# Optimization experiments

Hardware: AMD Instinct MI355X
Metric: run time of the kernel (lower is better)

Reference implementation:

```python
import jax, jax.numpy as jnp
import numpy as np

N_NODES = 65536
N_EDGES = 1048576
BN_EPS = 1e-5


def _glorot(key, shape):
    fan_in, fan_out = shape[0], shape[1]
    lim = np.sqrt(6.0 / (fan_in + fan_out))
    return jax.random.uniform(key, shape, jnp.float32, -lim, lim)


def setup_inputs() -> dict:
    key = jax.random.key(0)
    ks = jax.random.split(key, 16)
    inp = {}
    inp['x'] = jax.random.normal(ks[0], (N_NODES, 3), jnp.float32)
    inp['edge_src'] = jax.random.randint(ks[1], (N_EDGES,), 0, N_NODES, jnp.int32)
    inp['edge_dst'] = jax.random.randint(ks[2], (N_EDGES,), 0, N_NODES, jnp.int32)
    inp['edge_val'] = jax.random.uniform(ks[3], (N_EDGES,), jnp.float32)
    inp['num_pts'] = 1024  # points per shape (equal-size split)
    # GraphConvolution params: out = adj @ (x @ W) + b
    inp['gc1_w'] = _glorot(ks[4], (3, 64));     inp['gc1_b'] = jnp.zeros((64,), jnp.float32)
    inp['gc2_w'] = _glorot(ks[5], (64, 64));    inp['gc2_b'] = jnp.zeros((64,), jnp.float32)
    inp['gc3_w'] = _glorot(ks[6], (64, 1024));  inp['gc3_b'] = jnp.zeros((1024,), jnp.float32)
    # MLP head: Linear(1024,512)+BN+ReLU, Linear(512,256)+BN+ReLU, Linear(256,40)
    inp['fc1_w'] = _glorot(ks[7], (1024, 512)); inp['fc1_b'] = jnp.zeros((512,), jnp.float32)
    inp['bn1_g'] = jnp.ones((512,), jnp.float32); inp['bn1_b'] = jnp.zeros((512,), jnp.float32)
    inp['fc2_w'] = _glorot(ks[8], (512, 256));  inp['fc2_b'] = jnp.zeros((256,), jnp.float32)
    inp['bn2_g'] = jnp.ones((256,), jnp.float32); inp['bn2_b'] = jnp.zeros((256,), jnp.float32)
    inp['fc3_w'] = _glorot(ks[9], (256, 40));   inp['fc3_b'] = jnp.zeros((40,), jnp.float32)
    return inp


def _gcn_layer(x, w, b, src, dst, val):
    # adj @ (x @ W) + b, adj given as COO edge list (dst <- src weighted by val)
    support = x @ w                                   # [N, F_out]
    msg = support[src] * val[:, None]                 # gather + scale
    agg = jax.ops.segment_sum(msg, dst, num_segments=N_NODES)
    return agg + b


def _batchnorm(x, gamma, beta):
    mean = jnp.mean(x, axis=0)
    var = jnp.mean(jnp.square(x - mean), axis=0)  # biased var (torch train mode)
    return (x - mean) * jax.lax.rsqrt(var + BN_EPS) * gamma + beta


def reference(x, edge_src, edge_dst, edge_val, num_pts,
              gc1_w, gc1_b, gc2_w, gc2_b, gc3_w, gc3_b,
              fc1_w, fc1_b, bn1_g, bn1_b, fc2_w, fc2_b, bn2_g, bn2_b, fc3_w, fc3_b):
    h = jax.nn.relu(_gcn_layer(x, gc1_w, gc1_b, edge_src, edge_dst, edge_val))
    h = jax.nn.relu(_gcn_layer(h, gc2_w, gc2_b, edge_src, edge_dst, edge_val))
    h = jax.nn.relu(_gcn_layer(h, gc3_w, gc3_b, edge_src, edge_dst, edge_val))
    # per-shape max pool: split into equal-size shapes along node dim
    n_shapes = N_NODES // num_pts
    global_feat = jnp.max(h.reshape(n_shapes, num_pts, 1024), axis=1)  # [B, 1024]
    # MLP head with train-mode BatchNorm
    z = jax.nn.relu(_batchnorm(global_feat @ fc1_w + fc1_b, bn1_g, bn1_b))
    z = jax.nn.relu(_batchnorm(z @ fc2_w + fc2_b, bn2_g, bn2_b))
    scores = z @ fc3_w + fc3_b                         # [B, 40]
    return jax.nn.log_softmax(scores, axis=-1)
```

## Files before the change

### kernel.cpp

```cpp
#include <hip/hip_runtime.h>
#include <math.h>

#define NN 65536
#define NE 1048576
#define CAP 17408
#define PCAP 24576

typedef __attribute__((ext_vector_type(8))) short short8;
typedef __attribute__((ext_vector_type(4))) float f32x4;

__device__ inline unsigned short f2bf(float f) {
  unsigned u = __float_as_uint(f);
  unsigned r = u + 0x7fff + ((u >> 16) & 1);
  return (unsigned short)(r >> 16);
}
__device__ inline float bf2f(unsigned short h) { return __uint_as_float(((unsigned)h) << 16); }

__global__ __launch_bounds__(256) void k_prep(const float* __restrict__ x, float4* __restrict__ x4,
                                              int* __restrict__ gcur, const float* __restrict__ w3,
                                              unsigned short* __restrict__ bfrag, unsigned* __restrict__ gf) {
  int bid = blockIdx.x, tid = threadIdx.x;
  if (bid < 256) {
    if (bid == 0 && tid < 64) gcur[tid] = 0;
    int n = bid * 256 + tid;
    x4[n] = make_float4(x[3 * n], x[3 * n + 1], x[3 * n + 2], 0.f);
  } else {
    int t = (bid - 256) * 256 + tid;
    if (t < 65536) gf[t] = 0u;
    int e = t & 7, g = (t >> 3) & 3, col = (t >> 5) & 1023, q = t >> 15;
    int k = (q & 1) * 32 + g * 8 + e;
    float v = w3[k * 1024 + col];
    unsigned short hv = f2bf(v);
    bfrag[t] = (q < 2) ? hv : f2bf(v - bf2f(hv));
  }
}

__global__ __launch_bounds__(256) void k_bin(const int* __restrict__ src, const int* __restrict__ dst,
                                             const float* __restrict__ val, int* __restrict__ gcur,
                                             uint2* __restrict__ ebin) {
  __shared__ int cnt[64], base[64];
  int tid = threadIdx.x;
  if (tid < 64) cnt[tid] = 0;
  __syncthreads();
  int e0 = blockIdx.x * 4096;
  int rsrc[16], rdst[16], rrank[16];
  float rval[16];
#pragma unroll
  for (int i = 0; i < 16; ++i) {
    int e = e0 + i * 256 + tid;
    rsrc[i] = src[e];
    rdst[i] = dst[e];
    rval[i] = val[e];
    rrank[i] = atomicAdd(&cnt[rdst[i] >> 10], 1);
  }
  __syncthreads();
  if (tid < 64) base[tid] = atomicAdd(&gcur[tid], cnt[tid]);
  __syncthreads();
#pragma unroll
  for (int i = 0; i < 16; ++i) {
    int b = rdst[i] >> 10;
    ebin[b * CAP + base[b] + rrank[i]] =
        make_uint2((unsigned)rsrc[i] | ((unsigned)(rdst[i] & 1023) << 16), (unsigned)__float_as_int(rval[i]));
  }
}

__global__ __launch_bounds__(1024) void k_csr(const int* __restrict__ gcnt, const uint2* __restrict__ ebin,
                                              int2* __restrict__ offdeg, int2* __restrict__ pack) {
  __shared__ int lcnt[1024], lcur[1024], part[1024];
  int b = blockIdx.x, tid = threadIdx.x;
  int count = gcnt[b];
  int gbase = b * PCAP;
  lcnt[tid] = 0;
  __syncthreads();
  const uint2* eb = ebin + (size_t)b * CAP;
  for (int i0 = 0; i0 < count; i0 += 4096) {
    unsigned xs[4];
#pragma unroll
    for (int u = 0; u < 4; ++u) {
      int i = i0 + u * 1024 + tid;
      xs[u] = eb[min(i, count - 1)].x;
    }
#pragma unroll
    for (int u = 0; u < 4; ++u) {
      int i = i0 + u * 1024 + tid;
      if (i < count) atomicAdd(&lcnt[(xs[u] >> 16) & 1023], 1);
    }
  }
  __syncthreads();
  int deg = lcnt[tid];
  int pdeg = (deg + 7) & ~7;
  part[tid] = pdeg;
  __syncthreads();
  for (int d = 1; d < 1024; d <<= 1) {
    int v = (tid >= d) ? part[tid - d] : 0;
    __syncthreads();
    part[tid] += v;
    __syncthreads();
  }
  int o0 = part[tid] - pdeg;
  lcur[tid] = o0;
  offdeg[b * 1024 + tid] = make_int2(gbase + o0, pdeg);
  __syncthreads();
  for (int i0 = 0; i0 < count; i0 += 4096) {
    uint2 es[4];
#pragma unroll
    for (int u = 0; u < 4; ++u) {
      int i = i0 + u * 1024 + tid;
      es[u] = eb[min(i, count - 1)];
    }
#pragma unroll
    for (int u = 0; u < 4; ++u) {
      int i = i0 + u * 1024 + tid;
      if (i < count) {
        int ld = (es[u].x >> 16) & 1023;
        int p = atomicAdd(&lcur[ld], 1);
        pack[gbase + p] = make_int2((int)((es[u].x & 0xffffu) << 7), (int)es[u].y);
      }
    }
  }
  int pend = o0 + pdeg;
  for (int p = o0 + deg; p < pend; ++p) pack[gbase + p] = make_int2(0, 0);
}

__global__ __launch_bounds__(256) void k_aggx(const int2* __restrict__ offdeg, const int2* __restrict__ pack,
                                              const float4* __restrict__ x4, float* __restrict__ aggx) {
  int n = blockIdx.x * 256 + threadIdx.x;
  int2 od = offdeg[n];
  int i0 = od.x, pdeg = od.y;
  float a0 = 0.f, a1 = 0.f, a2 = 0.f;
  for (int b = 0; b < pdeg; b += 8) {
    int2 ed[8];
    float4 q[8];
#pragma unroll
    for (int u = 0; u < 8; ++u) ed[u] = pack[i0 + b + u];
#pragma unroll
    for (int u = 0; u < 8; ++u) q[u] = x4[(unsigned)ed[u].x >> 7];
#pragma unroll
    for (int u = 0; u < 8; ++u) {
      float v = __int_as_float(ed[u].y);
      a0 = fmaf(v, q[u].x, a0);
      a1 = fmaf(v, q[u].y, a1);
      a2 = fmaf(v, q[u].z, a2);
    }
  }
  aggx[n * 3 + 0] = a0;
  aggx[n * 3 + 1] = a1;
  aggx[n * 3 + 2] = a2;
}

__global__ __launch_bounds__(256) void k_gemm1(const float* __restrict__ aggx, const float* __restrict__ w,
                                               const float* __restrict__ b, unsigned short* __restrict__ out) {
  __shared__ float sw[256];
  int t = threadIdx.x;
  sw[t] = (t < 192) ? w[t] : b[t - 192];
  __syncthreads();
  int g = blockIdx.x * 256 + t;
  int n = g >> 6, j = g & 63;
  float a0 = aggx[n * 3], a1 = aggx[n * 3 + 1], a2 = aggx[n * 3 + 2];
  float r = sw[192 + j];
  r = fmaf(a0, sw[j], r);
  r = fmaf(a1, sw[64 + j], r);
  r = fmaf(a2, sw[128 + j], r);
  out[g] = f2bf(fmaxf(r, 0.f));
}

__global__ __launch_bounds__(256) void k_agg64g2(const int2* __restrict__ offdeg, const int2* __restrict__ pack,
                                                 const unsigned short* __restrict__ h,
                                                 const float* __restrict__ w2, const float* __restrict__ b2,
                                                 unsigned short* __restrict__ out) {
  __shared__ float sw[64][64];
  __shared__ float rows[32][64];
  int tid = threadIdx.x;
  int lane = tid & 63, wv = tid >> 6;
  for (int t = tid; t < 1024; t += 256) ((float4*)sw)[t] = ((const float4*)w2)[t];
  __syncthreads();
  int o = lane >> 3, fl = lane & 7;
  int n = blockIdx.x * 32 + wv * 8 + o;
  int2 od = offdeg[n];
  int i0 = od.x, pdeg = od.y;
  const char* hb = (const char*)h;
  unsigned fo = (unsigned)(fl << 4);
  float c0 = 0.f, c1 = 0.f, c2 = 0.f, c3 = 0.f, c4 = 0.f, c5 = 0.f, c6 = 0.f, c7 = 0.f;
  for (int b = 0; b < pdeg; b += 8) {
    int2 ed[8];
    uint4 hv[8];
#pragma unroll
    for (int u = 0; u < 8; ++u) ed[u] = pack[i0 + b + u];
#pragma unroll
    for (int u = 0; u < 8; ++u) hv[u] = *(const uint4*)(hb + ((unsigned)ed[u].x + fo));
#pragma unroll
    for (int u = 0; u < 8; ++u) {
      float v = __int_as_float(ed[u].y);
      c0 = fmaf(v, __uint_as_float(hv[u].x << 16), c0);
      c1 = fmaf(v, __uint_as_float(hv[u].x & 0xffff0000u), c1);
      c2 = fmaf(v, __uint_as_float(hv[u].y << 16), c2);
      c3 = fmaf(v, __uint_as_float(hv[u].y & 0xffff0000u), c3);
      c4 = fmaf(v, __uint_as_float(hv[u].z << 16), c4);
      c5 = fmaf(v, __uint_as_float(hv[u].z & 0xffff0000u), c5);
      c6 = fmaf(v, __uint_as_float(hv[u].w << 16), c6);
      c7 = fmaf(v, __uint_as_float(hv[u].w & 0xffff0000u), c7);
    }
  }
  ((float4*)rows[wv * 8 + o])[fl * 2 + 0] = make_float4(c0, c1, c2, c3);
  ((float4*)rows[wv * 8 + o])[fl * 2 + 1] = make_float4(c4, c5, c6, c7);
  int nA = blockIdx.x * 32 + wv * 8;
  float bb = b2[lane];
  float acc[8];
#pragma unroll
  for (int r = 0; r < 8; ++r) acc[r] = bb;
#pragma unroll
  for (int kk = 0; kk < 16; ++kk) {
    float w0 = sw[4 * kk + 0][lane], w1 = sw[4 * kk + 1][lane];
    float w2v = sw[4 * kk + 2][lane], w3v = sw[4 * kk + 3][lane];
#pragma unroll
    for (int r = 0; r < 8; ++r) {
      float4 qr = ((const float4*)rows[wv * 8 + r])[kk];
      acc[r] = fmaf(qr.x, w0, acc[r]);
      acc[r] = fmaf(qr.y, w1, acc[r]);
      acc[r] = fmaf(qr.z, w2v, acc[r]);
      acc[r] = fmaf(qr.w, w3v, acc[r]);
    }
  }
#pragma unroll
  for (int r = 0; r < 8; ++r)
    out[(size_t)(nA + r) * 64 + lane] = f2bf(fmaxf(acc[r], 0.f));
}

__global__ __launch_bounds__(256) void k_agg64_split(const int2* __restrict__ offdeg, const int2* __restrict__ pack,
                                                     const unsigned short* __restrict__ h,
                                                     unsigned short* __restrict__ hi,
                                                     unsigned short* __restrict__ lo) {
  int tid = threadIdx.x;
  int lane = tid & 63, wv = tid >> 6;
  int o = lane >> 3, fl = lane & 7;
  int n = blockIdx.x * 32 + wv * 8 + o;
  int2 od = offdeg[n];
  int i0 = od.x, pdeg = od.y;
  const char* hb = (const char*)h;
  unsigned fo = (unsigned)(fl << 4);
  float c0 = 0.f, c1 = 0.f, c2 = 0.f, c3 = 0.f, c4 = 0.f, c5 = 0.f, c6 = 0.f, c7 = 0.f;
  for (int b = 0; b < pdeg; b += 8) {
    int2 ed[8];
    uint4 hv[8];
#pragma unroll
    for (int u = 0; u < 8; ++u) ed[u] = pack[i0 + b + u];
#pragma unroll
    for (int u = 0; u < 8; ++u) hv[u] = *(const uint4*)(hb + ((unsigned)ed[u].x + fo));
#pragma unroll
    for (int u = 0; u < 8; ++u) {
      float v = __int_as_float(ed[u].y);
      c0 = fmaf(v, __uint_as_float(hv[u].x << 16), c0);
      c1 = fmaf(v, __uint_as_float(hv[u].x & 0xffff0000u), c1);
      c2 = fmaf(v, __uint_as_float(hv[u].y << 16), c2);
      c3 = fmaf(v, __uint_as_float(hv[u].y & 0xffff0000u), c3);
      c4 = fmaf(v, __uint_as_float(hv[u].z << 16), c4);
      c5 = fmaf(v, __uint_as_float(hv[u].z & 0xffff0000u), c5);
      c6 = fmaf(v, __uint_as_float(hv[u].w << 16), c6);
      c7 = fmaf(v, __uint_as_float(hv[u].w & 0xffff0000u), c7);
    }
  }
  unsigned short h0 = f2bf(c0), h1 = f2bf(c1), h2 = f2bf(c2), h3 = f2bf(c3);
  unsigned short h4 = f2bf(c4), h5 = f2bf(c5), h6 = f2bf(c6), h7 = f2bf(c7);
  uint4 hiw = make_uint4((unsigned)h0 | ((unsigned)h1 << 16), (unsigned)h2 | ((unsigned)h3 << 16),
                         (unsigned)h4 | ((unsigned)h5 << 16), (unsigned)h6 | ((unsigned)h7 << 16));
  unsigned short l0 = f2bf(c0 - bf2f(h0)), l1 = f2bf(c1 - bf2f(h1));
  unsigned short l2 = f2bf(c2 - bf2f(h2)), l3 = f2bf(c3 - bf2f(h3));
  unsigned short l4 = f2bf(c4 - bf2f(h4)), l5 = f2bf(c5 - bf2f(h5));
  unsigned short l6 = f2bf(c6 - bf2f(h6)), l7 = f2bf(c7 - bf2f(h7));
  uint4 low = make_uint4((unsigned)l0 | ((unsigned)l1 << 16), (unsigned)l2 | ((unsigned)l3 << 16),
                         (unsigned)l4 | ((unsigned)l5 << 16), (unsigned)l6 | ((unsigned)l7 << 16));
  ((uint4*)hi)[(size_t)n * 8 + fl] = hiw;
  ((uint4*)lo)[(size_t)n * 8 + fl] = low;
}

__global__ __launch_bounds__(512) void k_gemm3max(const unsigned short* __restrict__ Ahi,
                                                  const unsigned short* __restrict__ Alo,
                                                  const unsigned short* __restrict__ Bfrag,
                                                  const float* __restrict__ b3,
                                                  unsigned* __restrict__ gf) {
  int b = blockIdx.x;
  int colhalf = b & 1, rowchunk = b >> 1;
  int shape = rowchunk >> 2;
  int tid = threadIdx.x;
  int wv = tid >> 6, l = tid & 63;
  int g = l >> 4, lr = l & 15;

  const short8* bf = (const short8*)Bfrag;
  int c0 = colhalf * 512 + wv * 64 + lr;
  short8 B0[4], B1[4], B2[4], B3[4];
#pragma unroll
  for (int ct = 0; ct < 4; ++ct) {
    int col = c0 + ct * 16;
    B0[ct] = bf[(0 * 1024 + col) * 4 + g];
    B1[ct] = bf[(1 * 1024 + col) * 4 + g];
    B2[ct] = bf[(2 * 1024 + col) * 4 + g];
    B3[ct] = bf[(3 * 1024 + col) * 4 + g];
  }

  float m[4] = {-1e30f, -1e30f, -1e30f, -1e30f};
  size_t abase = ((size_t)rowchunk * 256 + lr) * 64 + g * 8;
  for (int t = 0; t < 16; ++t) {
    size_t o = abase + (size_t)t * 16 * 64;
    short8 ah0 = *(const short8*)(Ahi + o);
    short8 ah1 = *(const short8*)(Ahi + o + 32);
    short8 al0 = *(const short8*)(Alo + o);
    short8 al1 = *(const short8*)(Alo + o + 32);
#pragma unroll
    for (int ct = 0; ct < 4; ++ct) {
      f32x4 acc = {0.f, 0.f, 0.f, 0.f};
      acc = __builtin_amdgcn_mfma_f32_16x16x32_bf16(ah0, B0[ct], acc, 0, 0, 0);
      acc = __builtin_amdgcn_mfma_f32_16x16x32_bf16(ah1, B1[ct], acc, 0, 0, 0);
      acc = __builtin_amdgcn_mfma_f32_16x16x32_bf16(ah0, B2[ct], acc, 0, 0, 0);
      acc = __builtin_amdgcn_mfma_f32_16x16x32_bf16(ah1, B3[ct], acc, 0, 0, 0);
      acc = __builtin_amdgcn_mfma_f32_16x16x32_bf16(al0, B0[ct], acc, 0, 0, 0);
      acc = __builtin_amdgcn_mfma_f32_16x16x32_bf16(al1, B1[ct], acc, 0, 0, 0);
      m[ct] = fmaxf(m[ct], fmaxf(fmaxf(acc[0], acc[1]), fmaxf(acc[2], acc[3])));
    }
  }
#pragma unroll
  for (int ct = 0; ct < 4; ++ct) {
    float mm = m[ct];
    mm = fmaxf(mm, __shfl_xor(mm, 16));
    mm = fmaxf(mm, __shfl_xor(mm, 32));
    if (g == 0) {
      int col = c0 + ct * 16;
      float v = fmaxf(mm + b3[col], 0.f);
      atomicMax(&gf[shape * 1024 + col], __float_as_uint(v));
    }
  }
}

__global__ __launch_bounds__(512) void k_fc(const float* __restrict__ in, const float* __restrict__ w,
                                            const float* __restrict__ bias, float* __restrict__ out,
                                            int K, int J) {
  __shared__ float sin_[1024];
  __shared__ float part[8][64];
  int jt = blockIdx.x, bb = blockIdx.y;
  int tid = threadIdx.x, s = tid >> 6, lane = tid & 63;
  for (int i = tid; i < K; i += 512) sin_[i] = in[bb * K + i];
  __syncthreads();
  int j = (jt << 6) + lane;
  int Ks = K >> 3;
  int k0 = s * Ks;
  float acc = 0.f;
  for (int k = 0; k < Ks; k += 16) {
    float wv[16];
#pragma unroll
    for (int u = 0; u < 16; ++u) wv[u] = w[(k0 + k + u) * J + j];
#pragma unroll
    for (int u = 0; u < 16; ++u) acc = fmaf(sin_[k0 + k + u], wv[u], acc);
  }
  part[s][lane] = acc;
  __syncthreads();
  if (tid < 64) {
    float r = bias[(jt << 6) + tid];
#pragma unroll
    for (int u = 0; u < 8; ++u) r += part[u][tid];
    out[bb * J + (jt << 6) + tid] = r;
  }
}

__global__ __launch_bounds__(256) void k_bn(const float* __restrict__ z, const float* __restrict__ g,
                                            const float* __restrict__ bt, float* __restrict__ out, int J) {
  __shared__ float tile[64][64];
  __shared__ float red[4][64];
  __shared__ float sc[64], sh[64];
  int tid = threadIdx.x, s = tid >> 6, lane = tid & 63;
  int j0 = blockIdx.x << 6;
  float psum = 0.f;
#pragma unroll
  for (int r = 0; r < 16; ++r) {
    int row = s * 16 + r;
    float v = z[row * J + j0 + lane];
    tile[row][lane] = v;
    psum += v;
  }
  red[s][lane] = psum;
  __syncthreads();
  if (tid < 64) sc[tid] = (red[0][tid] + red[1][tid] + red[2][tid] + red[3][tid]) * (1.f / 64.f);
  __syncthreads();
  float mean = sc[lane];
  float pv = 0.f;
#pragma unroll
  for (int r = 0; r < 16; ++r) {
    float d = tile[s * 16 + r][lane] - mean;
    pv = fmaf(d, d, pv);
  }
  red[s][lane] = pv;
  __syncthreads();
  if (tid < 64) {
    float var = (red[0][tid] + red[1][tid] + red[2][tid] + red[3][tid]) * (1.f / 64.f);
    float scale = g[j0 + tid] / sqrtf(var + 1e-5f);
    sh[tid] = bt[j0 + tid] - sc[tid] * scale;
    sc[tid] = scale;
  }
  __syncthreads();
  float scale = sc[lane], shift = sh[lane];
#pragma unroll
  for (int r = 0; r < 16; ++r) {
    int row = s * 16 + r;
    out[row * J + j0 + lane] = fmaxf(fmaf(tile[row][lane], scale, shift), 0.f);
  }
}

__global__ __launch_bounds__(256) void k_head2(const float* __restrict__ z2, const float* __restrict__ g,
                                               const float* __restrict__ bt, const float* __restrict__ w,
                                               const float* __restrict__ b, float* __restrict__ out) {
  __shared__ float sz[256];
  __shared__ float part[4][64];
  int bb = blockIdx.x, j = threadIdx.x;
  float s = 0.f;
#pragma unroll 8
  for (int r = 0; r < 64; ++r) s += z2[r * 256 + j];
  float mean = s * (1.f / 64.f);
  float v = 0.f;
#pragma unroll 8
  for (int r = 0; r < 64; ++r) {
    float d = z2[r * 256 + j] - mean;
    v = fmaf(d, d, v);
  }
  float scale = g[j] / sqrtf(v * (1.f / 64.f) + 1e-5f);
  float shift = bt[j] - mean * scale;
  sz[j] = fmaxf(fmaf(z2[bb * 256 + j], scale, shift), 0.f);
  __syncthreads();
  int sgrp = j >> 6, lane = j & 63;
  float acc = 0.f;
  if (lane < 40) {
#pragma unroll
    for (int k = 0; k < 64; k += 4) {
      int kk = sgrp * 64 + k;
      acc = fmaf(sz[kk + 0], w[(kk + 0) * 40 + lane], acc);
      acc = fmaf(sz[kk + 1], w[(kk + 1) * 40 + lane], acc);
      acc = fmaf(sz[kk + 2], w[(kk + 2) * 40 + lane], acc);
      acc = fmaf(sz[kk + 3], w[(kk + 3) * 40 + lane], acc);
    }
  }
  part[sgrp][lane] = acc;
  __syncthreads();
  if (j < 64) {
    float lv = (j < 40) ? part[0][j] + part[1][j] + part[2][j] + part[3][j] + b[j] : -INFINITY;
    float m = lv;
    for (int d = 32; d > 0; d >>= 1) m = fmaxf(m, __shfl_xor(m, d));
    float e = (j < 40) ? expf(lv - m) : 0.f;
    for (int d = 32; d > 0; d >>= 1) e += __shfl_xor(e, d);
    if (j < 40) out[bb * 40 + j] = lv - m - logf(e);
  }
}

extern "C" void kernel_launch(void* const* d_in, const int* in_sizes, int n_in,
                              void* d_out, int out_size, void* d_ws, size_t ws_size,
                              hipStream_t stream) {
  (void)in_sizes; (void)n_in; (void)out_size; (void)ws_size;
  const float* x    = (const float*)d_in[0];
  const int*   esrc = (const int*)d_in[1];
  const int*   edst = (const int*)d_in[2];
  const float* ev   = (const float*)d_in[3];
  const float* gc1w = (const float*)d_in[5];
  const float* gc1b = (const float*)d_in[6];
  const float* gc2w = (const float*)d_in[7];
  const float* gc2b = (const float*)d_in[8];
  const float* gc3w = (const float*)d_in[9];
  const float* gc3b = (const float*)d_in[10];
  const float* fc1w = (const float*)d_in[11];
  const float* fc1b = (const float*)d_in[12];
  const float* bn1g = (const float*)d_in[13];
  const float* bn1b = (const float*)d_in[14];
  const float* fc2w = (const float*)d_in[15];
  const float* fc2b = (const float*)d_in[16];
  const float* bn2g = (const float*)d_in[17];
  const float* bn2b = (const float*)d_in[18];
  const float* fc3w = (const float*)d_in[19];
  const float* fc3b = (const float*)d_in[20];

  char* ws = (char*)d_ws;
  size_t o = 0;
  auto alloc = [&](size_t bytes) -> void* {
    void* p = ws + o;
    o += (bytes + 255) & ~(size_t)255;
    return p;
  };
  int2*  offdeg = (int2*)alloc((size_t)NN * 8);
  int*   gcur = (int*)alloc(64 * 4);
  int2*  pack = (int2*)alloc((size_t)64 * PCAP * 8);
  float* aggx = (float*)alloc((size_t)NN * 3 * 4);
  float4* x4  = (float4*)alloc((size_t)NN * 16);
  float* bufA = (float*)alloc((size_t)NN * 64 * 4);
  float* bufB = (float*)alloc((size_t)NN * 64 * 4);
  uint2* ebin = (uint2*)bufA;
  unsigned short* h1_16 = (unsigned short*)bufA;
  unsigned short* h2_16 = (unsigned short*)((char*)bufA + NN * 64 * 2);
  unsigned short* Ahi = (unsigned short*)bufB;
  unsigned short* Alo = (unsigned short*)(bufB + NN * 32);
  unsigned short* Bfrag = (unsigned short*)alloc(4 * 1024 * 32 * 2);
  float* gf   = (float*)alloc(64 * 1024 * 4);
  float* z1   = (float*)alloc(64 * 512 * 4);
  float* z1n  = (float*)alloc(64 * 512 * 4);
  float* z2   = (float*)alloc(64 * 256 * 4);

  k_prep<<<768, 256, 0, stream>>>(x, x4, gcur, gc3w, Bfrag, (unsigned*)gf);

  k_bin<<<NE / 4096, 256, 0, stream>>>(esrc, edst, ev, gcur, ebin);
  k_csr<<<64, 1024, 0, stream>>>(gcur, ebin, offdeg, pack);

  k_aggx<<<NN / 256, 256, 0, stream>>>(offdeg, pack, x4, aggx);
  k_gemm1<<<(NN * 64) / 256, 256, 0, stream>>>(aggx, gc1w, gc1b, h1_16);

  k_agg64g2<<<NN / 32, 256, 0, stream>>>(offdeg, pack, h1_16, gc2w, gc2b, h2_16);

  k_agg64_split<<<NN / 32, 256, 0, stream>>>(offdeg, pack, h2_16, Ahi, Alo);
  k_gemm3max<<<512, 512, 0, stream>>>(Ahi, Alo, Bfrag, gc3b, (unsigned*)gf);

  k_fc<<<dim3(8, 64), 512, 0, stream>>>(gf, fc1w, fc1b, z1, 1024, 512);
  k_bn<<<8, 256, 0, stream>>>(z1, bn1g, bn1b, z1n, 512);
  k_fc<<<dim3(4, 64), 512, 0, stream>>>(z1n, fc2w, fc2b, z2, 512, 256);
  k_head2<<<64, 256, 0, stream>>>(z2, bn2g, bn2b, fc3w, fc3b, (float*)d_out);
}
```

Before: 167.2 us.

## Fuse layer-1 aggregate+GEMM, merge MLP head into cooperative kernel, vectorize loads

Merges the layer-1 aggregation and its 3x64 transform into one kernel, which drops the aggx round-trip and one launch. The four MLP-head kernels become a single cooperative kernel that uses grid.sync between the FC and BatchNorm stages. It also vectorizes the edge loads in the binning kernel and the pack loads in the aggregation kernels, and replaces the block-wide shared-memory scan in the CSR kernel with a wave-shuffle scan. The cooperative launch adds grid-sync overhead and requires all 256 blocks to be co-resident.

```diff
diff --git a/kernel.cpp b/kernel.cpp
--- a/kernel.cpp
+++ b/kernel.cpp
@@ -1,5 +1,8 @@
 #include <hip/hip_runtime.h>
+#include <hip/hip_cooperative_groups.h>
 #include <math.h>
+
+namespace cg = cooperative_groups;
 
 #define NN 65536
 #define NE 1048576
@@ -43,15 +46,21 @@
   if (tid < 64) cnt[tid] = 0;
   __syncthreads();
   int e0 = blockIdx.x * 4096;
+  const int4* src4 = (const int4*)(src + e0);
+  const int4* dst4 = (const int4*)(dst + e0);
+  const float4* val4 = (const float4*)(val + e0);
   int rsrc[16], rdst[16], rrank[16];
   float rval[16];
 #pragma unroll
-  for (int i = 0; i < 16; ++i) {
-    int e = e0 + i * 256 + tid;
-    rsrc[i] = src[e];
-    rdst[i] = dst[e];
-    rval[i] = val[e];
-    rrank[i] = atomicAdd(&cnt[rdst[i] >> 10], 1);
+  for (int i = 0; i < 4; ++i) {
+    int4 s4 = src4[i * 256 + tid];
+    int4 d4 = dst4[i * 256 + tid];
+    float4 v4 = val4[i * 256 + tid];
+    rsrc[4 * i + 0] = s4.x; rsrc[4 * i + 1] = s4.y; rsrc[4 * i + 2] = s4.z; rsrc[4 * i + 3] = s4.w;
+    rdst[4 * i + 0] = d4.x; rdst[4 * i + 1] = d4.y; rdst[4 * i + 2] = d4.z; rdst[4 * i + 3] = d4.w;
+    rval[4 * i + 0] = v4.x; rval[4 * i + 1] = v4.y; rval[4 * i + 2] = v4.z; rval[4 * i + 3] = v4.w;
+#pragma unroll
+    for (int u = 0; u < 4; ++u) rrank[4 * i + u] = atomicAdd(&cnt[rdst[4 * i + u] >> 10], 1);
   }
   __syncthreads();
   if (tid < 64) base[tid] = atomicAdd(&gcur[tid], cnt[tid]);
@@ -66,7 +75,8 @@
 
 __global__ __launch_bounds__(1024) void k_csr(const int* __restrict__ gcnt, const uint2* __restrict__ ebin,
                                               int2* __restrict__ offdeg, int2* __restrict__ pack) {
-  __shared__ int lcnt[1024], lcur[1024], part[1024];
+  __shared__ int lcnt[1024], lcur[1024];
+  __shared__ int wsum[16], woff[16];
   int b = blockIdx.x, tid = threadIdx.x;
   int count = gcnt[b];
   int gbase = b * PCAP;
@@ -89,15 +99,27 @@
   __syncthreads();
   int deg = lcnt[tid];
   int pdeg = (deg + 7) & ~7;
-  part[tid] = pdeg;
-  __syncthreads();
-  for (int d = 1; d < 1024; d <<= 1) {
-    int v = (tid >= d) ? part[tid - d] : 0;
-    __syncthreads();
-    part[tid] += v;
-    __syncthreads();
-  }
-  int o0 = part[tid] - pdeg;
+  int lane = tid & 63, wid = tid >> 6;
+  int v = pdeg;
+#pragma unroll
+  for (int d = 1; d < 64; d <<= 1) {
+    int t = __shfl_up(v, d);
+    if (lane >= d) v += t;
+  }
+  if (lane == 63) wsum[wid] = v;
+  __syncthreads();
+  if (tid < 16) {
+    int s = wsum[tid];
+    int sv = s;
+#pragma unroll
+    for (int d = 1; d < 16; d <<= 1) {
+      int t = __shfl_up(sv, d);
+      if (tid >= d) sv += t;
+    }
+    woff[tid] = sv - s;
+  }
+  __syncthreads();
+  int o0 = woff[wid] + v - pdeg;
   lcur[tid] = o0;
   offdeg[b * 1024 + tid] = make_int2(gbase + o0, pdeg);
   __syncthreads();
@@ -122,46 +144,46 @@
   for (int p = o0 + deg; p < pend; ++p) pack[gbase + p] = make_int2(0, 0);
 }
 
-__global__ __launch_bounds__(256) void k_aggx(const int2* __restrict__ offdeg, const int2* __restrict__ pack,
-                                              const float4* __restrict__ x4, float* __restrict__ aggx) {
-  int n = blockIdx.x * 256 + threadIdx.x;
+__global__ __launch_bounds__(256) void k_agg1(const int2* __restrict__ offdeg, const int2* __restrict__ pack,
+                                              const float4* __restrict__ x4, const float* __restrict__ w,
+                                              const float* __restrict__ b, unsigned short* __restrict__ out) {
+  __shared__ float sw[256];
+  __shared__ float sa[256][4];
+  int tid = threadIdx.x;
+  sw[tid] = (tid < 192) ? w[tid] : b[tid - 192];
+  int n = blockIdx.x * 256 + tid;
   int2 od = offdeg[n];
   int i0 = od.x, pdeg = od.y;
   float a0 = 0.f, a1 = 0.f, a2 = 0.f;
-  for (int b = 0; b < pdeg; b += 8) {
-    int2 ed[8];
+  for (int bb = 0; bb < pdeg; bb += 8) {
+    int4 p0 = *(const int4*)&pack[i0 + bb];
+    int4 p1 = *(const int4*)&pack[i0 + bb + 2];
+    int4 p2 = *(const int4*)&pack[i0 + bb + 4];
+    int4 p3 = *(const int4*)&pack[i0 + bb + 6];
+    int sx[8] = {p0.x, p0.z, p1.x, p1.z, p2.x, p2.z, p3.x, p3.z};
+    int vv[8] = {p0.y, p0.w, p1.y, p1.w, p2.y, p2.w, p3.y, p3.w};
     float4 q[8];
 #pragma unroll
-    for (int u = 0; u < 8; ++u) ed[u] = pack[i0 + b + u];
-#pragma unroll
-    for (int u = 0; u < 8; ++u) q[u] = x4[(unsigned)ed[u].x >> 7];
+    for (int u = 0; u < 8; ++u) q[u] = x4[(unsigned)sx[u] >> 7];
 #pragma unroll
     for (int u = 0; u < 8; ++u) {
-      float v = __int_as_float(ed[u].y);
+      float v = __int_as_float(vv[u]);
       a0 = fmaf(v, q[u].x, a0);
       a1 = fmaf(v, q[u].y, a1);
       a2 = fmaf(v, q[u].z, a2);
     }
   }
-  aggx[n * 3 + 0] = a0;
-  aggx[n * 3 + 1] = a1;
-  aggx[n * 3 + 2] = a2;
-}
-
-__global__ __launch_bounds__(256) void k_gemm1(const float* __restrict__ aggx, const float* __restrict__ w,
-                                               const float* __restrict__ b, unsigned short* __restrict__ out) {
-  __shared__ float sw[256];
-  int t = threadIdx.x;
-  sw[t] = (t < 192) ? w[t] : b[t - 192];
-  __syncthreads();
-  int g = blockIdx.x * 256 + t;
-  int n = g >> 6, j = g & 63;
-  float a0 = aggx[n * 3], a1 = aggx[n * 3 + 1], a2 = aggx[n * 3 + 2];
-  float r = sw[192 + j];
-  r = fmaf(a0, sw[j], r);
-  r = fmaf(a1, sw[64 + j], r);
-  r = fmaf(a2, sw[128 + j], r);
-  out[g] = f2bf(fmaxf(r, 0.f));
+  sa[tid][0] = a0; sa[tid][1] = a1; sa[tid][2] = a2;
+  __syncthreads();
+  int j = tid & 63, g = tid >> 6;
+  float wj0 = sw[j], wj1 = sw[64 + j], wj2 = sw[128 + j], bj = sw[192 + j];
+  int nb = blockIdx.x * 256 + g * 64;
+  for (int r = 0; r < 64; ++r) {
+    float r0 = fmaf(sa[g * 64 + r][0], wj0, bj);
+    r0 = fmaf(sa[g * 64 + r][1], wj1, r0);
+    r0 = fmaf(sa[g * 64 + r][2], wj2, r0);
+    out[(size_t)(nb + r) * 64 + j] = f2bf(fmaxf(r0, 0.f));
+  }
 }
 
 __global__ __launch_bounds__(256) void k_agg64g2(const int2* __restrict__ offdeg, const int2* __restrict__ pack,
@@ -182,15 +204,18 @@
   unsigned fo = (unsigned)(fl << 4);
   float c0 = 0.f, c1 = 0.f, c2 = 0.f, c3 = 0.f, c4 = 0.f, c5 = 0.f, c6 = 0.f, c7 = 0.f;
   for (int b = 0; b < pdeg; b += 8) {
-    int2 ed[8];
+    int4 p0 = *(const int4*)&pack[i0 + b];
+    int4 p1 = *(const int4*)&pack[i0 + b + 2];
+    int4 p2 = *(const int4*)&pack[i0 + b + 4];
+    int4 p3 = *(const int4*)&pack[i0 + b + 6];
+    int sx[8] = {p0.x, p0.z, p1.x, p1.z, p2.x, p2.z, p3.x, p3.z};
+    int vv[8] = {p0.y, p0.w, p1.y, p1.w, p2.y, p2.w, p3.y, p3.w};
     uint4 hv[8];
 #pragma unroll
-    for (int u = 0; u < 8; ++u) ed[u] = pack[i0 + b + u];
-#pragma unroll
-    for (int u = 0; u < 8; ++u) hv[u] = *(const uint4*)(hb + ((unsigned)ed[u].x + fo));
+    for (int u = 0; u < 8; ++u) hv[u] = *(const uint4*)(hb + ((unsigned)sx[u] + fo));
 #pragma unroll
     for (int u = 0; u < 8; ++u) {
-      float v = __int_as_float(ed[u].y);
+      float v = __int_as_float(vv[u]);
       c0 = fmaf(v, __uint_as_float(hv[u].x << 16), c0);
       c1 = fmaf(v, __uint_as_float(hv[u].x & 0xffff0000u), c1);
       c2 = fmaf(v, __uint_as_float(hv[u].y << 16), c2);
@@ -240,15 +265,18 @@
   unsigned fo = (unsigned)(fl << 4);
   float c0 = 0.f, c1 = 0.f, c2 = 0.f, c3 = 0.f, c4 = 0.f, c5 = 0.f, c6 = 0.f, c7 = 0.f;
   for (int b = 0; b < pdeg; b += 8) {
-    int2 ed[8];
+    int4 p0 = *(const int4*)&pack[i0 + b];
+    int4 p1 = *(const int4*)&pack[i0 + b + 2];
+    int4 p2 = *(const int4*)&pack[i0 + b + 4];
+    int4 p3 = *(const int4*)&pack[i0 + b + 6];
+    int sx[8] = {p0.x, p0.z, p1.x, p1.z, p2.x, p2.z, p3.x, p3.z};
+    int vv[8] = {p0.y, p0.w, p1.y, p1.w, p2.y, p2.w, p3.y, p3.w};
     uint4 hv[8];
 #pragma unroll
-    for (int u = 0; u < 8; ++u) ed[u] = pack[i0 + b + u];
-#pragma unroll
-    for (int u = 0; u < 8; ++u) hv[u] = *(const uint4*)(hb + ((unsigned)ed[u].x + fo));
+    for (int u = 0; u < 8; ++u) hv[u] = *(const uint4*)(hb + ((unsigned)sx[u] + fo));
 #pragma unroll
     for (int u = 0; u < 8; ++u) {
-      float v = __int_as_float(ed[u].y);
+      float v = __int_as_float(vv[u]);
       c0 = fmaf(v, __uint_as_float(hv[u].x << 16), c0);
       c1 = fmaf(v, __uint_as_float(hv[u].x & 0xffff0000u), c1);
       c2 = fmaf(v, __uint_as_float(hv[u].y << 16), c2);
@@ -330,120 +358,132 @@
   }
 }
 
-__global__ __launch_bounds__(512) void k_fc(const float* __restrict__ in, const float* __restrict__ w,
-                                            const float* __restrict__ bias, float* __restrict__ out,
-                                            int K, int J) {
-  __shared__ float sin_[1024];
-  __shared__ float part[8][64];
-  int jt = blockIdx.x, bb = blockIdx.y;
-  int tid = threadIdx.x, s = tid >> 6, lane = tid & 63;
-  for (int i = tid; i < K; i += 512) sin_[i] = in[bb * K + i];
-  __syncthreads();
-  int j = (jt << 6) + lane;
-  int Ks = K >> 3;
-  int k0 = s * Ks;
-  float acc = 0.f;
-  for (int k = 0; k < Ks; k += 16) {
-    float wv[16];
-#pragma unroll
-    for (int u = 0; u < 16; ++u) wv[u] = w[(k0 + k + u) * J + j];
-#pragma unroll
-    for (int u = 0; u < 16; ++u) acc = fmaf(sin_[k0 + k + u], wv[u], acc);
-  }
-  part[s][lane] = acc;
-  __syncthreads();
+__global__ __launch_bounds__(256) void k_mlp(const float* __restrict__ gf, const float* __restrict__ w1,
+                                             const float* __restrict__ b1, const float* __restrict__ g1,
+                                             const float* __restrict__ be1, const float* __restrict__ w2,
+                                             const float* __restrict__ b2, const float* __restrict__ g2,
+                                             const float* __restrict__ be2, const float* __restrict__ w3,
+                                             const float* __restrict__ b3, float* __restrict__ z1,
+                                             float* __restrict__ z2, float* __restrict__ sc1,
+                                             float* __restrict__ sh1, float* __restrict__ sc2,
+                                             float* __restrict__ sh2, float* __restrict__ out) {
+  cg::grid_group grid = cg::this_grid();
+  __shared__ float sbuf[2][1024];
+  __shared__ float part[256];
+  int b = blockIdx.x, tid = threadIdx.x;
+
+  {
+    int jt = b & 7, r0 = (b >> 3) * 2;
+    for (int i = tid; i < 2048; i += 256)
+      sbuf[i >> 10][i & 1023] = gf[(r0 + (i >> 10)) * 1024 + (i & 1023)];
+    __syncthreads();
+    int j = tid & 63, rr = (tid >> 6) & 1, hh = tid >> 7;
+    const float* srow = sbuf[rr];
+    int k0 = hh * 512;
+    float acc = 0.f;
+    for (int k = 0; k < 512; k += 16) {
+      float wv[16];
+#pragma unroll
+      for (int u = 0; u < 16; ++u) wv[u] = w1[(k0 + k + u) * 512 + jt * 64 + j];
+#pragma unroll
+      for (int u = 0; u < 16; ++u) acc = fmaf(srow[k0 + k + u], wv[u], acc);
+    }
+    part[tid] = acc;
+    __syncthreads();
+    if (tid < 128) {
+      int jj = jt * 64 + (tid & 63);
+      z1[(r0 + ((tid >> 6) & 1)) * 512 + jj] = part[tid] + part[tid + 128] + b1[jj];
+    }
+  }
+  grid.sync();
+  if (tid < 128) {
+    int c = 2 * b + (tid >> 6);
+    int lane = tid & 63;
+    float xv = z1[lane * 512 + c];
+    float s = xv;
+#pragma unroll
+    for (int d = 32; d > 0; d >>= 1) s += __shfl_xor(s, d);
+    float mean = s * (1.f / 64.f);
+    float dd = xv - mean;
+    float vv = dd * dd;
+#pragma unroll
+    for (int d = 32; d > 0; d >>= 1) vv += __shfl_xor(vv, d);
+    if (lane == 0) {
+      float scale = g1[c] / sqrtf(vv * (1.f / 64.f) + 1e-5f);
+      sc1[c] = scale;
+      sh1[c] = be1[c] - mean * scale;
+    }
+  }
+  grid.sync();
+  {
+    int jt2 = b & 3, row = b >> 2;
+    float* szn = sbuf[0];
+    for (int i = tid; i < 512; i += 256)
+      szn[i] = fmaxf(fmaf(z1[row * 512 + i], sc1[i], sh1[i]), 0.f);
+    __syncthreads();
+    int j = tid & 63, q = tid >> 6;
+    int k0 = q * 128;
+    float acc = 0.f;
+    for (int k = 0; k < 128; k += 16) {
+      float wv[16];
+#pragma unroll
+      for (int u = 0; u < 16; ++u) wv[u] = w2[(k0 + k + u) * 256 + jt2 * 64 + j];
+#pragma unroll
+      for (int u = 0; u < 16; ++u) acc = fmaf(szn[k0 + k + u], wv[u], acc);
+    }
+    part[tid] = acc;
+    __syncthreads();
+    if (tid < 64) {
+      int jj = jt2 * 64 + tid;
+      z2[row * 256 + jj] = part[tid] + part[tid + 64] + part[tid + 128] + part[tid + 192] + b2[jj];
+    }
+    __syncthreads();
+  }
+  grid.sync();
   if (tid < 64) {
-    float r = bias[(jt << 6) + tid];
-#pragma unroll
-    for (int u = 0; u < 8; ++u) r += part[u][tid];
-    out[bb * J + (jt << 6) + tid] = r;
-  }
-}
-
-__global__ __launch_bounds__(256) void k_bn(const float* __restrict__ z, const float* __restrict__ g,
-                                            const float* __restrict__ bt, float* __restrict__ out, int J) {
-  __shared__ float tile[64][64];
-  __shared__ float red[4][64];
-  __shared__ float sc[64], sh[64];
-  int tid = threadIdx.x, s = tid >> 6, lane = tid & 63;
-  int j0 = blockIdx.x << 6;
-  float psum = 0.f;
-#pragma unroll
-  for (int r = 0; r < 16; ++r) {
-    int row = s * 16 + r;
-    float v = z[row * J + j0 + lane];
-    tile[row][lane] = v;
-    psum += v;
-  }
-  red[s][lane] = psum;
-  __syncthreads();
-  if (tid < 64) sc[tid] = (red[0][tid] + red[1][tid] + red[2][tid] + red[3][tid]) * (1.f / 64.f);
-  __syncthreads();
-  float mean = sc[lane];
-  float pv = 0.f;
-#pragma unroll
-  for (int r = 0; r < 16; ++r) {
-    float d = tile[s * 16 + r][lane] - mean;
-    pv = fmaf(d, d, pv);
-  }
-  red[s][lane] = pv;
-  __syncthreads();
-  if (tid < 64) {
-    float var = (red[0][tid] + red[1][tid] + red[2][tid] + red[3][tid]) * (1.f / 64.f);
-    float scale = g[j0 + tid] / sqrtf(var + 1e-5f);
-    sh[tid] = bt[j0 + tid] - sc[tid] * scale;
-    sc[tid] = scale;
-  }
-  __syncthreads();
-  float scale = sc[lane], shift = sh[lane];
-#pragma unroll
-  for (int r = 0; r < 16; ++r) {
-    int row = s * 16 + r;
-    out[row * J + j0 + lane] = fmaxf(fmaf(tile[row][lane], scale, shift), 0.f);
-  }
-}
-
-__global__ __launch_bounds__(256) void k_head2(const float* __restrict__ z2, const float* __restrict__ g,
-                                               const float* __restrict__ bt, const float* __restrict__ w,
-                                               const float* __restrict__ b, float* __restrict__ out) {
-  __shared__ float sz[256];
-  __shared__ float part[4][64];
-  int bb = blockIdx.x, j = threadIdx.x;
-  float s = 0.f;
-#pragma unroll 8
-  for (int r = 0; r < 64; ++r) s += z2[r * 256 + j];
-  float mean = s * (1.f / 64.f);
-  float v = 0.f;
-#pragma unroll 8
-  for (int r = 0; r < 64; ++r) {
-    float d = z2[r * 256 + j] - mean;
-    v = fmaf(d, d, v);
-  }
-  float scale = g[j] / sqrtf(v * (1.f / 64.f) + 1e-5f);
-  float shift = bt[j] - mean * scale;
-  sz[j] = fmaxf(fmaf(z2[bb * 256 + j], scale, shift), 0.f);
-  __syncthreads();
-  int sgrp = j >> 6, lane = j & 63;
-  float acc = 0.f;
-  if (lane < 40) {
-#pragma unroll
-    for (int k = 0; k < 64; k += 4) {
-      int kk = sgrp * 64 + k;
-      acc = fmaf(sz[kk + 0], w[(kk + 0) * 40 + lane], acc);
-      acc = fmaf(sz[kk + 1], w[(kk + 1) * 40 + lane], acc);
-      acc = fmaf(sz[kk + 2], w[(kk + 2) * 40 + lane], acc);
-      acc = fmaf(sz[kk + 3], w[(kk + 3) * 40 + lane], acc);
-    }
-  }
-  part[sgrp][lane] = acc;
-  __syncthreads();
-  if (j < 64) {
-    float lv = (j < 40) ? part[0][j] + part[1][j] + part[2][j] + part[3][j] + b[j] : -INFINITY;
-    float m = lv;
-    for (int d = 32; d > 0; d >>= 1) m = fmaxf(m, __shfl_xor(m, d));
-    float e = (j < 40) ? expf(lv - m) : 0.f;
-    for (int d = 32; d > 0; d >>= 1) e += __shfl_xor(e, d);
-    if (j < 40) out[bb * 40 + j] = lv - m - logf(e);
+    float xv = z2[tid * 256 + b];
+    float s = xv;
+#pragma unroll
+    for (int d = 32; d > 0; d >>= 1) s += __shfl_xor(s, d);
+    float mean = s * (1.f / 64.f);
+    float dd = xv - mean;
+    float vv = dd * dd;
+#pragma unroll
+    for (int d = 32; d > 0; d >>= 1) vv += __shfl_xor(vv, d);
+    if (tid == 0) {
+      float scale = g2[b] / sqrtf(vv * (1.f / 64.f) + 1e-5f);
+      sc2[b] = scale;
+      sh2[b] = be2[b] - mean * scale;
+    }
+  }
+  grid.sync();
+  if (b < 64) {
+    float* sz = sbuf[0];
+    sz[tid] = fmaxf(fmaf(z2[b * 256 + tid], sc2[tid], sh2[tid]), 0.f);
+    __syncthreads();
+    int sgrp = tid >> 6, lane = tid & 63;
+    float acc = 0.f;
+    if (lane < 40) {
+#pragma unroll
+      for (int k = 0; k < 64; k += 4) {
+        int kk = sgrp * 64 + k;
+        acc = fmaf(sz[kk + 0], w3[(kk + 0) * 40 + lane], acc);
+        acc = fmaf(sz[kk + 1], w3[(kk + 1) * 40 + lane], acc);
+        acc = fmaf(sz[kk + 2], w3[(kk + 2) * 40 + lane], acc);
+        acc = fmaf(sz[kk + 3], w3[(kk + 3) * 40 + lane], acc);
+      }
+    }
+    part[tid] = acc;
+    __syncthreads();
+    if (tid < 64) {
+      float lv = (tid < 40) ? part[tid] + part[64 + tid] + part[128 + tid] + part[192 + tid] + b3[tid]
+                            : -INFINITY;
+      float m = lv;
+      for (int d = 32; d > 0; d >>= 1) m = fmaxf(m, __shfl_xor(m, d));
+      float e = (tid < 40) ? expf(lv - m) : 0.f;
+      for (int d = 32; d > 0; d >>= 1) e += __shfl_xor(e, d);
+      if (tid < 40) out[b * 40 + tid] = lv - m - logf(e);
+    }
   }
 }
 
@@ -482,7 +522,6 @@
   int2*  offdeg = (int2*)alloc((size_t)NN * 8);
   int*   gcur = (int*)alloc(64 * 4);
   int2*  pack = (int2*)alloc((size_t)64 * PCAP * 8);
-  float* aggx = (float*)alloc((size_t)NN * 3 * 4);
   float4* x4  = (float4*)alloc((size_t)NN * 16);
   float* bufA = (float*)alloc((size_t)NN * 64 * 4);
   float* bufB = (float*)alloc((size_t)NN * 64 * 4);
@@ -494,24 +533,28 @@
   unsigned short* Bfrag = (unsigned short*)alloc(4 * 1024 * 32 * 2);
   float* gf   = (float*)alloc(64 * 1024 * 4);
   float* z1   = (float*)alloc(64 * 512 * 4);
-  float* z1n  = (float*)alloc(64 * 512 * 4);
   float* z2   = (float*)alloc(64 * 256 * 4);
+  float* sc1  = (float*)alloc(512 * 4);
+  float* sh1  = (float*)alloc(512 * 4);
+  float* sc2  = (float*)alloc(256 * 4);
+  float* sh2  = (float*)alloc(256 * 4);
 
   k_prep<<<768, 256, 0, stream>>>(x, x4, gcur, gc3w, Bfrag, (unsigned*)gf);
 
   k_bin<<<NE / 4096, 256, 0, stream>>>(esrc, edst, ev, gcur, ebin);
   k_csr<<<64, 1024, 0, stream>>>(gcur, ebin, offdeg, pack);
 
-  k_aggx<<<NN / 256, 256, 0, stream>>>(offdeg, pack, x4, aggx);
-  k_gemm1<<<(NN * 64) / 256, 256, 0, stream>>>(aggx, gc1w, gc1b, h1_16);
+  k_agg1<<<NN / 256, 256, 0, stream>>>(offdeg, pack, x4, gc1w, gc1b, h1_16);
 
   k_agg64g2<<<NN / 32, 256, 0, stream>>>(offdeg, pack, h1_16, gc2w, gc2b, h2_16);
 
   k_agg64_split<<<NN / 32, 256, 0, stream>>>(offdeg, pack, h2_16, Ahi, Alo);
   k_gemm3max<<<512, 512, 0, stream>>>(Ahi, Alo, Bfrag, gc3b, (unsigned*)gf);
 
-  k_fc<<<dim3(8, 64), 512, 0, stream>>>(gf, fc1w, fc1b, z1, 1024, 512);
-  k_bn<<<8, 256, 0, stream>>>(z1, bn1g, bn1b, z1n, 512);
-  k_fc<<<dim3(4, 64), 512, 0, stream>>>(z1n, fc2w, fc2b, z2, 512, 256);
-  k_head2<<<64, 256, 0, stream>>>(z2, bn2g, bn2b, fc3w, fc3b, (float*)d_out);
-}
+  float* outp = (float*)d_out;
+  void* kargs[] = {(void*)&gf,   (void*)&fc1w, (void*)&fc1b, (void*)&bn1g, (void*)&bn1b,
+                   (void*)&fc2w, (void*)&fc2b, (void*)&bn2g, (void*)&bn2b, (void*)&fc3w,
+                   (void*)&fc3b, (void*)&z1,   (void*)&z2,   (void*)&sc1,  (void*)&sh1,
+                   (void*)&sc2,  (void*)&sh2,  (void*)&outp};
+  hipLaunchCooperativeKernel((void*)k_mlp, dim3(256), dim3(256), kargs, 0, stream);
+}
```

Measured after the change: 267.8 us. 60.2% more time.

## Fuse layer-1 aggregate and GEMM, vectorise edge loads, warp-shuffle CSR scan

Applied to the files above, without the earlier changes.

Merges the layer-1 edge aggregation and its 3x64 projection into one kernel, which removes the aggx intermediate buffer and one launch. Edge loads in k_bin and in the three aggregation kernels are widened to 128-bit vector loads, so two packed edges are read per load. The 1024-wide prefix sum in k_csr now uses wavefront shuffles plus a small cross-wave pass in place of a shared-memory Hillis-Steele scan with many barriers. The fused kernel's output loop has each thread write 64 rows serially, which could limit parallelism in that phase.

```diff
diff --git a/kernel.cpp b/kernel.cpp
--- a/kernel.cpp
+++ b/kernel.cpp
@@ -43,15 +43,21 @@
   if (tid < 64) cnt[tid] = 0;
   __syncthreads();
   int e0 = blockIdx.x * 4096;
+  const int4* src4 = (const int4*)(src + e0);
+  const int4* dst4 = (const int4*)(dst + e0);
+  const float4* val4 = (const float4*)(val + e0);
   int rsrc[16], rdst[16], rrank[16];
   float rval[16];
 #pragma unroll
-  for (int i = 0; i < 16; ++i) {
-    int e = e0 + i * 256 + tid;
-    rsrc[i] = src[e];
-    rdst[i] = dst[e];
-    rval[i] = val[e];
-    rrank[i] = atomicAdd(&cnt[rdst[i] >> 10], 1);
+  for (int i = 0; i < 4; ++i) {
+    int4 s4 = src4[i * 256 + tid];
+    int4 d4 = dst4[i * 256 + tid];
+    float4 v4 = val4[i * 256 + tid];
+    rsrc[4 * i + 0] = s4.x; rsrc[4 * i + 1] = s4.y; rsrc[4 * i + 2] = s4.z; rsrc[4 * i + 3] = s4.w;
+    rdst[4 * i + 0] = d4.x; rdst[4 * i + 1] = d4.y; rdst[4 * i + 2] = d4.z; rdst[4 * i + 3] = d4.w;
+    rval[4 * i + 0] = v4.x; rval[4 * i + 1] = v4.y; rval[4 * i + 2] = v4.z; rval[4 * i + 3] = v4.w;
+#pragma unroll
+    for (int u = 0; u < 4; ++u) rrank[4 * i + u] = atomicAdd(&cnt[rdst[4 * i + u] >> 10], 1);
   }
   __syncthreads();
   if (tid < 64) base[tid] = atomicAdd(&gcur[tid], cnt[tid]);
@@ -66,7 +72,8 @@
 
 __global__ __launch_bounds__(1024) void k_csr(const int* __restrict__ gcnt, const uint2* __restrict__ ebin,
                                               int2* __restrict__ offdeg, int2* __restrict__ pack) {
-  __shared__ int lcnt[1024], lcur[1024], part[1024];
+  __shared__ int lcnt[1024], lcur[1024];
+  __shared__ int wsum[16], woff[16];
   int b = blockIdx.x, tid = threadIdx.x;
   int count = gcnt[b];
   int gbase = b * PCAP;
@@ -89,15 +96,27 @@
   __syncthreads();
   int deg = lcnt[tid];
   int pdeg = (deg + 7) & ~7;
-  part[tid] = pdeg;
-  __syncthreads();
-  for (int d = 1; d < 1024; d <<= 1) {
-    int v = (tid >= d) ? part[tid - d] : 0;
-    __syncthreads();
-    part[tid] += v;
-    __syncthreads();
-  }
-  int o0 = part[tid] - pdeg;
+  int lane = tid & 63, wid = tid >> 6;
+  int v = pdeg;
+#pragma unroll
+  for (int d = 1; d < 64; d <<= 1) {
+    int t = __shfl_up(v, d);
+    if (lane >= d) v += t;
+  }
+  if (lane == 63) wsum[wid] = v;
+  __syncthreads();
+  if (tid < 16) {
+    int s = wsum[tid];
+    int sv = s;
+#pragma unroll
+    for (int d = 1; d < 16; d <<= 1) {
+      int t = __shfl_up(sv, d);
+      if (tid >= d) sv += t;
+    }
+    woff[tid] = sv - s;
+  }
+  __syncthreads();
+  int o0 = woff[wid] + v - pdeg;
   lcur[tid] = o0;
   offdeg[b * 1024 + tid] = make_int2(gbase + o0, pdeg);
   __syncthreads();
@@ -122,46 +141,46 @@
   for (int p = o0 + deg; p < pend; ++p) pack[gbase + p] = make_int2(0, 0);
 }
 
-__global__ __launch_bounds__(256) void k_aggx(const int2* __restrict__ offdeg, const int2* __restrict__ pack,
-                                              const float4* __restrict__ x4, float* __restrict__ aggx) {
-  int n = blockIdx.x * 256 + threadIdx.x;
+__global__ __launch_bounds__(256) void k_agg1(const int2* __restrict__ offdeg, const int2* __restrict__ pack,
+                                              const float4* __restrict__ x4, const float* __restrict__ w,
+                                              const float* __restrict__ b, unsigned short* __restrict__ out) {
+  __shared__ float sw[256];
+  __shared__ float sa[256][4];
+  int tid = threadIdx.x;
+  sw[tid] = (tid < 192) ? w[tid] : b[tid - 192];
+  int n = blockIdx.x * 256 + tid;
   int2 od = offdeg[n];
   int i0 = od.x, pdeg = od.y;
   float a0 = 0.f, a1 = 0.f, a2 = 0.f;
-  for (int b = 0; b < pdeg; b += 8) {
-    int2 ed[8];
+  for (int bb = 0; bb < pdeg; bb += 8) {
+    int4 p0 = *(const int4*)&pack[i0 + bb];
+    int4 p1 = *(const int4*)&pack[i0 + bb + 2];
+    int4 p2 = *(const int4*)&pack[i0 + bb + 4];
+    int4 p3 = *(const int4*)&pack[i0 + bb + 6];
+    int sx[8] = {p0.x, p0.z, p1.x, p1.z, p2.x, p2.z, p3.x, p3.z};
+    int vv[8] = {p0.y, p0.w, p1.y, p1.w, p2.y, p2.w, p3.y, p3.w};
     float4 q[8];
 #pragma unroll
-    for (int u = 0; u < 8; ++u) ed[u] = pack[i0 + b + u];
-#pragma unroll
-    for (int u = 0; u < 8; ++u) q[u] = x4[(unsigned)ed[u].x >> 7];
+    for (int u = 0; u < 8; ++u) q[u] = x4[(unsigned)sx[u] >> 7];
 #pragma unroll
     for (int u = 0; u < 8; ++u) {
-      float v = __int_as_float(ed[u].y);
+      float v = __int_as_float(vv[u]);
       a0 = fmaf(v, q[u].x, a0);
       a1 = fmaf(v, q[u].y, a1);
       a2 = fmaf(v, q[u].z, a2);
     }
   }
-  aggx[n * 3 + 0] = a0;
-  aggx[n * 3 + 1] = a1;
-  aggx[n * 3 + 2] = a2;
-}
-
-__global__ __launch_bounds__(256) void k_gemm1(const float* __restrict__ aggx, const float* __restrict__ w,
-                                               const float* __restrict__ b, unsigned short* __restrict__ out) {
-  __shared__ float sw[256];
-  int t = threadIdx.x;
-  sw[t] = (t < 192) ? w[t] : b[t - 192];
-  __syncthreads();
-  int g = blockIdx.x * 256 + t;
-  int n = g >> 6, j = g & 63;
-  float a0 = aggx[n * 3], a1 = aggx[n * 3 + 1], a2 = aggx[n * 3 + 2];
-  float r = sw[192 + j];
-  r = fmaf(a0, sw[j], r);
-  r = fmaf(a1, sw[64 + j], r);
-  r = fmaf(a2, sw[128 + j], r);
-  out[g] = f2bf(fmaxf(r, 0.f));
+  sa[tid][0] = a0; sa[tid][1] = a1; sa[tid][2] = a2;
+  __syncthreads();
+  int j = tid & 63, g = tid >> 6;
+  float wj0 = sw[j], wj1 = sw[64 + j], wj2 = sw[128 + j], bj = sw[192 + j];
+  int nb = blockIdx.x * 256 + g * 64;
+  for (int r = 0; r < 64; ++r) {
+    float r0 = fmaf(sa[g * 64 + r][0], wj0, bj);
+    r0 = fmaf(sa[g * 64 + r][1], wj1, r0);
+    r0 = fmaf(sa[g * 64 + r][2], wj2, r0);
+    out[(size_t)(nb + r) * 64 + j] = f2bf(fmaxf(r0, 0.f));
+  }
 }
 
 __global__ __launch_bounds__(256) void k_agg64g2(const int2* __restrict__ offdeg, const int2* __restrict__ pack,
@@ -182,15 +201,18 @@
   unsigned fo = (unsigned)(fl << 4);
   float c0 = 0.f, c1 = 0.f, c2 = 0.f, c3 = 0.f, c4 = 0.f, c5 = 0.f, c6 = 0.f, c7 = 0.f;
   for (int b = 0; b < pdeg; b += 8) {
-    int2 ed[8];
+    int4 p0 = *(const int4*)&pack[i0 + b];
+    int4 p1 = *(const int4*)&pack[i0 + b + 2];
+    int4 p2 = *(const int4*)&pack[i0 + b + 4];
+    int4 p3 = *(const int4*)&pack[i0 + b + 6];
+    int sx[8] = {p0.x, p0.z, p1.x, p1.z, p2.x, p2.z, p3.x, p3.z};
+    int vv[8] = {p0.y, p0.w, p1.y, p1.w, p2.y, p2.w, p3.y, p3.w};
     uint4 hv[8];
 #pragma unroll
-    for (int u = 0; u < 8; ++u) ed[u] = pack[i0 + b + u];
-#pragma unroll
-    for (int u = 0; u < 8; ++u) hv[u] = *(const uint4*)(hb + ((unsigned)ed[u].x + fo));
+    for (int u = 0; u < 8; ++u) hv[u] = *(const uint4*)(hb + ((unsigned)sx[u] + fo));
 #pragma unroll
     for (int u = 0; u < 8; ++u) {
-      float v = __int_as_float(ed[u].y);
+      float v = __int_as_float(vv[u]);
       c0 = fmaf(v, __uint_as_float(hv[u].x << 16), c0);
       c1 = fmaf(v, __uint_as_float(hv[u].x & 0xffff0000u), c1);
       c2 = fmaf(v, __uint_as_float(hv[u].y << 16), c2);
@@ -240,15 +262,18 @@
   unsigned fo = (unsigned)(fl << 4);
   float c0 = 0.f, c1 = 0.f, c2 = 0.f, c3 = 0.f, c4 = 0.f, c5 = 0.f, c6 = 0.f, c7 = 0.f;
   for (int b = 0; b < pdeg; b += 8) {
-    int2 ed[8];
+    int4 p0 = *(const int4*)&pack[i0 + b];
+    int4 p1 = *(const int4*)&pack[i0 + b + 2];
+    int4 p2 = *(const int4*)&pack[i0 + b + 4];
+    int4 p3 = *(const int4*)&pack[i0 + b + 6];
+    int sx[8] = {p0.x, p0.z, p1.x, p1.z, p2.x, p2.z, p3.x, p3.z};
+    int vv[8] = {p0.y, p0.w, p1.y, p1.w, p2.y, p2.w, p3.y, p3.w};
     uint4 hv[8];
 #pragma unroll
-    for (int u = 0; u < 8; ++u) ed[u] = pack[i0 + b + u];
-#pragma unroll
-    for (int u = 0; u < 8; ++u) hv[u] = *(const uint4*)(hb + ((unsigned)ed[u].x + fo));
+    for (int u = 0; u < 8; ++u) hv[u] = *(const uint4*)(hb + ((unsigned)sx[u] + fo));
 #pragma unroll
     for (int u = 0; u < 8; ++u) {
-      float v = __int_as_float(ed[u].y);
+      float v = __int_as_float(vv[u]);
       c0 = fmaf(v, __uint_as_float(hv[u].x << 16), c0);
       c1 = fmaf(v, __uint_as_float(hv[u].x & 0xffff0000u), c1);
       c2 = fmaf(v, __uint_as_float(hv[u].y << 16), c2);
@@ -482,7 +507,6 @@
   int2*  offdeg = (int2*)alloc((size_t)NN * 8);
   int*   gcur = (int*)alloc(64 * 4);
   int2*  pack = (int2*)alloc((size_t)64 * PCAP * 8);
-  float* aggx = (float*)alloc((size_t)NN * 3 * 4);
   float4* x4  = (float4*)alloc((size_t)NN * 16);
   float* bufA = (float*)alloc((size_t)NN * 64 * 4);
   float* bufB = (float*)alloc((size_t)NN * 64 * 4);
@@ -502,8 +526,7 @@
   k_bin<<<NE / 4096, 256, 0, stream>>>(esrc, edst, ev, gcur, ebin);
   k_csr<<<64, 1024, 0, stream>>>(gcur, ebin, offdeg, pack);
 
-  k_aggx<<<NN / 256, 256, 0, stream>>>(offdeg, pack, x4, aggx);
-  k_gemm1<<<(NN * 64) / 256, 256, 0, stream>>>(aggx, gc1w, gc1b, h1_16);
+  k_agg1<<<NN / 256, 256, 0, stream>>>(offdeg, pack, x4, gc1w, gc1b, h1_16);
 
   k_agg64g2<<<NN / 32, 256, 0, stream>>>(offdeg, pack, h1_16, gc2w, gc2b, h2_16);
 
```

Result: faster. 159.4 us (-4.7%).
